# Performance work log

Measured on AMD Instinct MI355X. Metric: run time of the kernel, lower is better.

## Reference

```python
import jax, jax.numpy as jnp
import numpy as np

N, E, D, H, C = 20000, 320000, 128, 4, 128
NEG_SLOPE = 0.2

def _ln(x, g, b, eps=1e-5):
    mu = x.mean(-1, keepdims=True)
    var = ((x - mu) ** 2).mean(-1, keepdims=True)
    return (x - mu) * jax.lax.rsqrt(var + eps) * g + b

def _gatv2(x, src, dst, Wl, bl, Wr, br, att, b):
    # PyG GATv2Conv, concat=False (mean over heads), dropout off (eval)
    n = x.shape[0]
    xl = (x @ Wl + bl).reshape(n, H, C)   # source transform
    xr = (x @ Wr + br).reshape(n, H, C)   # destination transform
    e = jax.nn.leaky_relu(xl[src] + xr[dst], NEG_SLOPE)      # [E,H,C]
    score = jnp.einsum('ehc,hc->eh', e, att)                 # [E,H]
    m = jax.ops.segment_max(score, dst, num_segments=n)      # per-dst max
    w = jnp.exp(score - m[dst])
    denom = jax.ops.segment_sum(w, dst, num_segments=n)
    alpha = w / (denom[dst] + 1e-16)                         # softmax over incoming edges
    out = jax.ops.segment_sum(alpha[:, :, None] * xl[src], dst, num_segments=n)  # [N,H,C]
    return out.mean(axis=1) + b

def setup_inputs() -> dict:
    key = jax.random.key(0)
    ks = jax.random.split(key, 34)
    s = 1.0 / np.sqrt(D)
    def w(k, shape):
        return jax.random.normal(k, shape, jnp.float32) * s
    inp = {
        'x': jax.random.normal(ks[0], (N, D), jnp.float32),
        'edge_index': jax.random.randint(ks[1], (2, E), 0, N, jnp.int32),
        'W_in': w(ks[2], (D, C)), 'b_in': jnp.zeros((C,), jnp.float32),
        'c1_Wl': w(ks[3], (C, H * C)), 'c1_bl': jnp.zeros((H * C,), jnp.float32),
        'c1_Wr': w(ks[4], (C, H * C)), 'c1_br': jnp.zeros((H * C,), jnp.float32),
        'c1_att': w(ks[5], (H, C)), 'c1_b': jnp.zeros((C,), jnp.float32),
        'ln1_g': jnp.ones((C,), jnp.float32), 'ln1_b': jnp.zeros((C,), jnp.float32),
        'a_Wl': w(ks[6], (C, H * C)), 'a_bl': jnp.zeros((H * C,), jnp.float32),
        'a_Wr': w(ks[7], (C, H * C)), 'a_br': jnp.zeros((H * C,), jnp.float32),
        'a_att': w(ks[8], (H, C)), 'a_b': jnp.zeros((C,), jnp.float32),
        'aln_g': jnp.ones((C,), jnp.float32), 'aln_b': jnp.zeros((C,), jnp.float32),
        'ah_W': w(ks[9], (C, 1)), 'ah_b': jnp.zeros((1,), jnp.float32),
        'k_Wl': w(ks[10], (C, H * C)), 'k_bl': jnp.zeros((H * C,), jnp.float32),
        'k_Wr': w(ks[11], (C, H * C)), 'k_br': jnp.zeros((H * C,), jnp.float32),
        'k_att': w(ks[12], (H, C)), 'k_b': jnp.zeros((C,), jnp.float32),
        'kln_g': jnp.ones((C,), jnp.float32), 'kln_b': jnp.zeros((C,), jnp.float32),
        'kh_W': w(ks[13], (C, 1)), 'kh_b': jnp.zeros((1,), jnp.float32),
    }
    return inp

def reference(x, edge_index, W_in, b_in,
              c1_Wl, c1_bl, c1_Wr, c1_br, c1_att, c1_b, ln1_g, ln1_b,
              a_Wl, a_bl, a_Wr, a_br, a_att, a_b, aln_g, aln_b, ah_W, ah_b,
              k_Wl, k_bl, k_Wr, k_br, k_att, k_b, kln_g, kln_b, kh_W, kh_b):
    n = x.shape[0]
    loops = jnp.arange(n, dtype=edge_index.dtype)
    src = jnp.concatenate([edge_index[0], loops])  # PyG adds self-loops by default
    dst = jnp.concatenate([edge_index[1], loops])
    h = jax.nn.relu(x @ W_in + b_in)
    h_res = _gatv2(h, src, dst, c1_Wl, c1_bl, c1_Wr, c1_br, c1_att, c1_b)
    h = jax.nn.relu(_ln(h + h_res, ln1_g, ln1_b))
    xa = _gatv2(h, src, dst, a_Wl, a_bl, a_Wr, a_br, a_att, a_b)
    xa = jax.nn.relu(_ln(xa + h, aln_g, aln_b))
    action_logits = (xa @ ah_W + ah_b).squeeze(-1)
    xc = _gatv2(h, src, dst, k_Wl, k_bl, k_Wr, k_br, k_att, k_b)
    xc = jax.nn.relu(_ln(xc + h, kln_g, kln_b))
    state_value = xc @ kh_W + kh_b
    return action_logits, state_value
```

## Files before the change

### kernel.cpp

```cpp
#include <hip/hip_runtime.h>
#include <hip/hip_bf16.h>

typedef __hip_bfloat16 bf16;
typedef __attribute__((ext_vector_type(8))) short short8;
typedef __attribute__((ext_vector_type(4))) short short4_t;
typedef __attribute__((ext_vector_type(4))) float float4_t;
typedef __attribute__((ext_vector_type(2))) float float2v;
typedef __attribute__((ext_vector_type(2))) unsigned int uint2v;

__device__ __forceinline__ short f2bs(float f) {
    bf16 b = __float2bfloat16(f);
    return *(short*)&b;
}

template <int CTRL>
__device__ __forceinline__ float dpp_addf(float x) {
    int s = __builtin_amdgcn_update_dpp(
        0, __builtin_bit_cast(int, x), CTRL, 0xf, 0xf, true);
    return x + __builtin_bit_cast(float, s);
}
__device__ __forceinline__ float rowsum16(float x) {
    x = dpp_addf<0xB1>(x);
    x = dpp_addf<0x4E>(x);
    x = dpp_addf<0x141>(x);
    x = dpp_addf<0x140>(x);
    return x;
}

__global__ __launch_bounds__(256) void zero_kernel(int* __restrict__ a, int n) {
    int i = blockIdx.x * 256 + threadIdx.x;
    if (i < n) a[i] = 0;
}

__global__ __launch_bounds__(256) void count_kernel(const int* __restrict__ ei,
                                                    int* __restrict__ cnt, int E, int N) {
    int e = blockIdx.x * 256 + threadIdx.x;
    if (e >= E + N) return;
    int d = (e < E) ? ei[(size_t)E + e] : (e - E);
    atomicAdd(&cnt[d], 1);
}

__global__ __launch_bounds__(1024) void scan_kernel(const int* __restrict__ cnt,
                                                    int* __restrict__ rowptr, int N) {
    __shared__ int ps[1024];
    const int tid = threadIdx.x;
    const int chunk = (N + 1023) / 1024;
    const int base = tid * chunk;
    int s = 0;
    for (int i = 0; i < chunk; ++i) { int j = base + i; if (j < N) s += cnt[j]; }
    ps[tid] = s;
    __syncthreads();
    for (int off = 1; off < 1024; off <<= 1) {
        int v = (tid >= off) ? ps[tid - off] : 0;
        __syncthreads();
        ps[tid] += v;
        __syncthreads();
    }
    int run = (tid == 0) ? 0 : ps[tid - 1];
    for (int i = 0; i < chunk; ++i) {
        int j = base + i;
        if (j < N) { rowptr[j] = run; run += cnt[j]; }
    }
    if (tid == 1023) rowptr[N] = run;
}

__global__ __launch_bounds__(256) void scatter_kernel(const int* __restrict__ ei,
                                                      const int* __restrict__ rowptr,
                                                      int* __restrict__ cursor,
                                                      int* __restrict__ csr_off,
                                                      int E, int N) {
    int e = blockIdx.x * 256 + threadIdx.x;
    if (e >= E + N) return;
    int s, d;
    if (e < E) { s = ei[e]; d = ei[(size_t)E + e]; }
    else       { s = e - E; d = e - E; }
    int pos = atomicAdd(&cursor[d], 1);
    csr_off[rowptr[d] + pos] = s * 4096;
}

__global__ __launch_bounds__(256) void transpose_w_kernel(
        const float* __restrict__ W_in,
        const float* __restrict__ c1_Wl, const float* __restrict__ c1_Wr,
        const float* __restrict__ a_Wl, const float* __restrict__ a_Wr,
        const float* __restrict__ k_Wl, const float* __restrict__ k_Wr,
        bf16* __restrict__ Wt) {
    __shared__ float tile[32][33];
    const float* src; int nc, drow;
    switch (blockIdx.z) {
        case 0: src = W_in;  nc = 128; drow = 0;    break;
        case 1: src = c1_Wl; nc = 512; drow = 128;  break;
        case 2: src = c1_Wr; nc = 512; drow = 640;  break;
        case 3: src = a_Wl;  nc = 512; drow = 1152; break;
        case 4: src = a_Wr;  nc = 512; drow = 1664; break;
        case 5: src = k_Wl;  nc = 512; drow = 2176; break;
        default: src = k_Wr; nc = 512; drow = 2688; break;
    }
    const int n0 = blockIdx.x * 32;
    if (n0 >= nc) return;
    const int k0 = blockIdx.y * 32;
    const int tx = threadIdx.x & 31, ty = threadIdx.x >> 5;
#pragma unroll
    for (int i = 0; i < 4; ++i)
        tile[ty + i * 8][tx] = src[(size_t)(k0 + ty + i * 8) * nc + n0 + tx];
    __syncthreads();
#pragma unroll
    for (int i = 0; i < 4; ++i)
        Wt[(size_t)(drow + n0 + ty + i * 8) * 128 + k0 + tx] =
            __float2bfloat16(tile[tx][ty + i * 8]);
}

__global__ __launch_bounds__(256) void bias_kernel(
        const float* __restrict__ c1_bl, const float* __restrict__ c1_br,
        const float* __restrict__ a_bl, const float* __restrict__ a_br,
        const float* __restrict__ k_bl, const float* __restrict__ k_br,
        float* __restrict__ b1, float* __restrict__ bak) {
    int i = blockIdx.x * 256 + threadIdx.x;
    if (i < 1024) {
        b1[i] = (i < 512) ? c1_bl[i] : c1_br[i - 512];
    } else if (i < 3072) {
        int j = i - 1024;
        const float* b = (j < 512) ? a_bl : (j < 1024) ? a_br : (j < 1536) ? k_bl : k_br;
        bak[j] = b[j & 511];
    }
}

__global__ __launch_bounds__(256, 2) void gemm_mfma_kernel(
        const float* __restrict__ A, const bf16* __restrict__ Ab,
        const bf16* __restrict__ Wt,
        const float* __restrict__ bias,
        float* __restrict__ outF, bf16* __restrict__ outB,
        int M, int ldc, int relu) {
    __shared__ short As[128][136];
    __shared__ short Bs[128][136];
    const int tid = threadIdx.x;
    const int m0 = blockIdx.x * 128;
    const int n0 = blockIdx.y * 128;

    if (Ab) {
        short8 zero8;
#pragma unroll
        for (int q = 0; q < 8; ++q) zero8[q] = 0;
#pragma unroll
        for (int i = 0; i < 8; ++i) {
            int idx = i * 256 + tid;
            int r = idx >> 4, k8 = (idx & 15) * 8;
            int gm = m0 + r;
            short8 s = (gm < M) ? *(const short8*)&Ab[(size_t)gm * 128 + k8] : zero8;
            *(short8*)&As[r][k8] = s;
        }
    } else {
#pragma unroll
        for (int i = 0; i < 16; ++i) {
            int idx = i * 256 + tid;
            int r = idx >> 5, k4 = (idx & 31) * 4;
            int gm = m0 + r;
            float4 v = (gm < M) ? *(const float4*)&A[(size_t)gm * 128 + k4]
                                : make_float4(0.f, 0.f, 0.f, 0.f);
            short4_t s;
            s.x = f2bs(v.x); s.y = f2bs(v.y); s.z = f2bs(v.z); s.w = f2bs(v.w);
            *(short4_t*)&As[r][k4] = s;
        }
    }
#pragma unroll
    for (int i = 0; i < 8; ++i) {
        int idx = i * 256 + tid;
        int nr = idx >> 4, k8 = (idx & 15) * 8;
        *(short8*)&Bs[nr][k8] = *(const short8*)&Wt[(size_t)(n0 + nr) * 128 + k8];
    }
    __syncthreads();

    const int lane = tid & 63;
    const int w = tid >> 6;
    const int wm = (w >> 1) * 64, wn = (w & 1) * 64;
    const int fr = lane & 15;
    const int fq = (lane >> 4) * 8;

    float4_t acc[4][4] = {};
#pragma unroll
    for (int kk = 0; kk < 128; kk += 32) {
        short8 a[4], b[4];
#pragma unroll
        for (int t = 0; t < 4; ++t) a[t] = *(const short8*)&As[wm + t * 16 + fr][kk + fq];
#pragma unroll
        for (int t = 0; t < 4; ++t) b[t] = *(const short8*)&Bs[wn + t * 16 + fr][kk + fq];
#pragma unroll
        for (int ti = 0; ti < 4; ++ti)
#pragma unroll
            for (int tj = 0; tj < 4; ++tj)
                acc[ti][tj] = __builtin_amdgcn_mfma_f32_16x16x32_bf16(
                    a[ti], b[tj], acc[ti][tj], 0, 0, 0);
    }

    const int r0 = (lane >> 4) * 4;
#pragma unroll
    for (int ti = 0; ti < 4; ++ti) {
#pragma unroll
        for (int tj = 0; tj < 4; ++tj) {
            int col = n0 + wn + tj * 16 + fr;
            float bz = bias[col];
#pragma unroll
            for (int r = 0; r < 4; ++r) {
                size_t row = m0 + wm + ti * 16 + r0 + r;
                float v = acc[ti][tj][r] + bz;
                if (relu) v = fmaxf(v, 0.f);
                if (outF) outF[row * ldc + col] = v;
                if (outB) outB[row * ldc + col] = __float2bfloat16(v);
            }
        }
    }
}

__global__ __launch_bounds__(256) void gat_kernel(
        const bf16* __restrict__ xl, const bf16* __restrict__ xr,
        const float* __restrict__ att,
        const int* __restrict__ rowptr, const int* __restrict__ csr_off,
        const float* __restrict__ h_res,
        const float* __restrict__ gbias,
        const float* __restrict__ ln_g, const float* __restrict__ ln_b,
        float* __restrict__ h_out, bf16* __restrict__ h_outb,
        const float* __restrict__ head_W, const float* __restrict__ head_b,
        float* __restrict__ out_scalar, int mode, int N) {
    const int n = blockIdx.x * 4 + (threadIdx.x >> 6);
    if (n >= N) return;
    const int lane = threadIdx.x & 63;
    const int sl = lane & 15;
    const int hc = (lane >> 4) * 128 + sl * 8;

    float2v c1[4], c2[4], xr2[4];
    {
        const float* ap = att + hc;
        short8 v = *(const short8*)(xr + (size_t)n * 2048 + hc);
        const unsigned int* uv = (const unsigned int*)&v;
#pragma unroll
        for (int j = 0; j < 4; ++j) {
            float a0 = ap[2 * j], a1 = ap[2 * j + 1];
            c1[j].x = 0.6f * a0; c1[j].y = 0.6f * a1;
            c2[j].x = 0.4f * a0; c2[j].y = 0.4f * a1;
            unsigned u = uv[j];
            xr2[j].x = __uint_as_float(u << 16);
            xr2[j].y = __uint_as_float(u & 0xffff0000u);
        }
    }
    const int rs = rowptr[n], re = rowptr[n + 1];
    const char* xlh = (const char*)xl + (size_t)hc * 2;

    float l = 0.f;
    float2v acc2[4] = {};
    int o0 = csr_off[rs];
    short8 va = *(const short8*)(xlh + o0);
    int o1 = (rs + 1 < re) ? csr_off[rs + 1] : o0;
    short8 vb = *(const short8*)(xlh + o1);
    int o2 = (rs + 2 < re) ? csr_off[rs + 2] : o0;

    for (int e = rs; e < re; ++e) {
        short8 cur = va; va = vb;
        if (e + 2 < re) {
            vb = *(const short8*)(xlh + o2);
            o2 = (e + 3 < re) ? csr_off[e + 3] : o0;
        }
        const unsigned int* uv = (const unsigned int*)&cur;
        float2v pa = {0.f, 0.f}, pb = {0.f, 0.f};
        float2v xs[4];
#pragma unroll
        for (int j = 0; j < 4; ++j) {
            unsigned u = uv[j];
            float2v x;
            x.x = __uint_as_float(u << 16);
            x.y = __uint_as_float(u & 0xffff0000u);
            xs[j] = x;
            float2v t = x + xr2[j];
            float2v ta = __builtin_bit_cast(float2v,
                           __builtin_bit_cast(uint2v, t) & 0x7fffffffu);
            pa = __builtin_elementwise_fma(c1[j], t, pa);
            pb = __builtin_elementwise_fma(c2[j], ta, pb);
        }
        float p = rowsum16((pa.x + pb.x) + (pa.y + pb.y));
        float wv = __expf(fminf(p, 60.f));
        l += wv;
        float2v ws = {wv, wv};
#pragma unroll
        for (int j = 0; j < 4; ++j)
            acc2[j] = __builtin_elementwise_fma(ws, xs[j], acc2[j]);
    }

    float* accf = (float*)acc2;
    const float inv = 0.25f / (l + 1e-16f);
#pragma unroll
    for (int j = 0; j < 8; ++j) accf[j] *= inv;
#pragma unroll
    for (int off = 16; off <= 32; off <<= 1)
#pragma unroll
        for (int j = 0; j < 8; ++j) accf[j] += __shfl_xor(accf[j], off, 64);

    if (lane < 16) {
        const int cb = sl * 8;
        const float* hr = h_res + (size_t)n * 128 + cb;
        float vv[8];
#pragma unroll
        for (int j = 0; j < 8; ++j) vv[j] = accf[j] + gbias[cb + j] + hr[j];
        float t1 = 0.f, t2 = 0.f;
#pragma unroll
        for (int j = 0; j < 8; ++j) { t1 += vv[j]; t2 += vv[j] * vv[j]; }
        const float s1 = rowsum16(t1), s2 = rowsum16(t2);
        const float mu   = s1 * 0.0078125f;
        const float var  = s2 * 0.0078125f - mu * mu;
        const float rstd = rsqrtf(var + 1e-5f);
        float y[8];
#pragma unroll
        for (int j = 0; j < 8; ++j) {
            y[j] = fmaf((vv[j] - mu) * rstd, ln_g[cb + j], ln_b[cb + j]);
            y[j] = fmaxf(y[j], 0.f);
        }
        if (mode == 0) {
            float4 y0 = make_float4(y[0], y[1], y[2], y[3]);
            float4 y1 = make_float4(y[4], y[5], y[6], y[7]);
            *(float4*)(h_out + (size_t)n * 128 + cb) = y0;
            *(float4*)(h_out + (size_t)n * 128 + cb + 4) = y1;
            short8 yb;
#pragma unroll
            for (int j = 0; j < 8; ++j) yb[j] = f2bs(y[j]);
            *(short8*)(h_outb + (size_t)n * 128 + cb) = yb;
        } else {
            float d = 0.f;
#pragma unroll
            for (int j = 0; j < 8; ++j) d += y[j] * head_W[cb + j];
            d = rowsum16(d);
            if (lane == 0) out_scalar[n] = d + head_b[0];
        }
    }
}

extern "C" void kernel_launch(void* const* d_in, const int* in_sizes, int n_in,
                              void* d_out, int out_size, void* d_ws, size_t ws_size,
                              hipStream_t stream) {
    const float* x      = (const float*)d_in[0];
    const int*   ei     = (const int*)  d_in[1];
    const float* W_in   = (const float*)d_in[2];
    const float* b_in   = (const float*)d_in[3];
    const float* c1_Wl  = (const float*)d_in[4];
    const float* c1_bl  = (const float*)d_in[5];
    const float* c1_Wr  = (const float*)d_in[6];
    const float* c1_br  = (const float*)d_in[7];
    const float* c1_att = (const float*)d_in[8];
    const float* c1_b   = (const float*)d_in[9];
    const float* ln1_g  = (const float*)d_in[10];
    const float* ln1_b  = (const float*)d_in[11];
    const float* a_Wl   = (const float*)d_in[12];
    const float* a_bl   = (const float*)d_in[13];
    const float* a_Wr   = (const float*)d_in[14];
    const float* a_br   = (const float*)d_in[15];
    const float* a_att  = (const float*)d_in[16];
    const float* a_b    = (const float*)d_in[17];
    const float* aln_g  = (const float*)d_in[18];
    const float* aln_b  = (const float*)d_in[19];
    const float* ah_W   = (const float*)d_in[20];
    const float* ah_b   = (const float*)d_in[21];
    const float* k_Wl   = (const float*)d_in[22];
    const float* k_bl   = (const float*)d_in[23];
    const float* k_Wr   = (const float*)d_in[24];
    const float* k_br   = (const float*)d_in[25];
    const float* k_att  = (const float*)d_in[26];
    const float* k_b    = (const float*)d_in[27];
    const float* kln_g  = (const float*)d_in[28];
    const float* kln_b  = (const float*)d_in[29];
    const float* kh_W   = (const float*)d_in[30];
    const float* kh_b   = (const float*)d_in[31];

    const int N  = in_sizes[0] / 128;
    const int E  = in_sizes[1] / 2;
    const int ET = E + N;
    const int MB = (N + 127) / 128;
    const int Npad = MB * 128;

    char* ws = (char*)d_ws;
    size_t off = 0;
    auto alloc = [&](size_t bytes) -> void* {
        void* p = ws + off;
        off += (bytes + 255) & ~(size_t)255;
        return p;
    };
    int*   rowptr  = (int*)alloc((size_t)(N + 1) * 4);
    int*   cntcur  = (int*)alloc((size_t)2 * N * 4);
    int*   csr_off = (int*)alloc((size_t)ET * 4);
    float* h0      = (float*)alloc((size_t)Npad * 128 * 4);
    bf16*  h0b     = (bf16*)alloc((size_t)Npad * 128 * 2);
    float* h1      = (float*)alloc((size_t)Npad * 128 * 4);
    bf16*  h1b     = (bf16*)alloc((size_t)Npad * 128 * 2);
    bf16*  Wt      = (bf16*)alloc((size_t)3200 * 128 * 2);
    float* b1cat   = (float*)alloc(1024 * 4);
    float* bakcat  = (float*)alloc(2048 * 4);
    bf16*  cat     = (bf16*)alloc((size_t)Npad * 2048 * 2);

    int* cnt    = cntcur;
    int* cursor = cntcur + N;
    const bf16* Wt_in = Wt;
    const bf16* Wt_1  = Wt + 128 * 128;
    const bf16* Wt_ak = Wt + 128 * 128 + 1024 * 128;

    float* out_logits = (float*)d_out;
    float* out_value  = (float*)d_out + N;

    zero_kernel<<<(2 * N + 255) / 256, 256, 0, stream>>>(cntcur, 2 * N);
    count_kernel<<<(ET + 255) / 256, 256, 0, stream>>>(ei, cnt, E, N);
    transpose_w_kernel<<<dim3(16, 4, 7), 256, 0, stream>>>(
        W_in, c1_Wl, c1_Wr, a_Wl, a_Wr, k_Wl, k_Wr, Wt);
    bias_kernel<<<12, 256, 0, stream>>>(c1_bl, c1_br, a_bl, a_br, k_bl, k_br, b1cat, bakcat);
    scan_kernel<<<1, 1024, 0, stream>>>(cnt, rowptr, N);
    scatter_kernel<<<(ET + 255) / 256, 256, 0, stream>>>(ei, rowptr, cursor, csr_off, E, N);

    gemm_mfma_kernel<<<dim3(MB, 1), 256, 0, stream>>>(x, nullptr, Wt_in, b_in,
                                                      h0, h0b, N, 128, 1);
    gemm_mfma_kernel<<<dim3(MB, 8), 256, 0, stream>>>(nullptr, h0b, Wt_1, b1cat,
                                                      nullptr, cat, Npad, 2048, 0);
    gat_kernel<<<(N + 3) / 4, 256, 0, stream>>>(cat, cat + 512, c1_att, rowptr, csr_off,
                                      h0, c1_b, ln1_g, ln1_b, h1, h1b,
                                      nullptr, nullptr, nullptr, 0, N);
    gemm_mfma_kernel<<<dim3(MB, 16), 256, 0, stream>>>(nullptr, h1b, Wt_ak, bakcat,
                                                       nullptr, cat, Npad, 2048, 0);
    gat_kernel<<<(N + 3) / 4, 256, 0, stream>>>(cat, cat + 512, a_att, rowptr, csr_off,
                                      h1, a_b, aln_g, aln_b, nullptr, nullptr,
                                      ah_W, ah_b, out_logits, 1, N);
    gat_kernel<<<(N + 3) / 4, 256, 0, stream>>>(cat + 1024, cat + 1536, k_att, rowptr, csr_off,
                                      h1, k_b, kln_g, kln_b, nullptr, nullptr,
                                      kh_W, kh_b, out_value, 1, N);
}
```

Measured before the change: 419.6 us.

## Fuse actor and critic GAT aggregations into one kernel sharing CSR traversal

Replaces the two separate actor and critic GAT launches with a single gat2 kernel. It walks each node's incoming edges once, gathering both the actor and critic source features and running both softmax aggregations plus their LayerNorm and heads. It also folds the bias-concat kernel into the weight-transpose launch and simplifies the leaky-ReLU coefficient math. The aim is to cut the repeated CSR and h_res reads and one launch, at the cost of roughly double register pressure per thread in the fused loop.

```diff
diff --git a/kernel.cpp b/kernel.cpp
--- a/kernel.cpp
+++ b/kernel.cpp
@@ -83,7 +83,25 @@
         const float* __restrict__ c1_Wl, const float* __restrict__ c1_Wr,
         const float* __restrict__ a_Wl, const float* __restrict__ a_Wr,
         const float* __restrict__ k_Wl, const float* __restrict__ k_Wr,
-        bf16* __restrict__ Wt) {
+        bf16* __restrict__ Wt,
+        const float* __restrict__ c1_bl, const float* __restrict__ c1_br,
+        const float* __restrict__ a_bl, const float* __restrict__ a_br,
+        const float* __restrict__ k_bl, const float* __restrict__ k_br,
+        float* __restrict__ b1, float* __restrict__ bak) {
+    if (blockIdx.z == 7) {
+        int flat = blockIdx.y * 16 + blockIdx.x;
+        if (flat >= 12) return;
+        int i = flat * 256 + threadIdx.x;
+        if (i < 1024) {
+            b1[i] = (i < 512) ? c1_bl[i] : c1_br[i - 512];
+        } else if (i < 3072) {
+            int j = i - 1024;
+            const float* b = (j < 512) ? a_bl : (j < 1024) ? a_br
+                           : (j < 1536) ? k_bl : k_br;
+            bak[j] = b[j & 511];
+        }
+        return;
+    }
     __shared__ float tile[32][33];
     const float* src; int nc, drow;
     switch (blockIdx.z) {
@@ -107,21 +125,6 @@
     for (int i = 0; i < 4; ++i)
         Wt[(size_t)(drow + n0 + ty + i * 8) * 128 + k0 + tx] =
             __float2bfloat16(tile[tx][ty + i * 8]);
-}
-
-__global__ __launch_bounds__(256) void bias_kernel(
-        const float* __restrict__ c1_bl, const float* __restrict__ c1_br,
-        const float* __restrict__ a_bl, const float* __restrict__ a_br,
-        const float* __restrict__ k_bl, const float* __restrict__ k_br,
-        float* __restrict__ b1, float* __restrict__ bak) {
-    int i = blockIdx.x * 256 + threadIdx.x;
-    if (i < 1024) {
-        b1[i] = (i < 512) ? c1_bl[i] : c1_br[i - 512];
-    } else if (i < 3072) {
-        int j = i - 1024;
-        const float* b = (j < 512) ? a_bl : (j < 1024) ? a_br : (j < 1536) ? k_bl : k_br;
-        bak[j] = b[j & 511];
-    }
 }
 
 __global__ __launch_bounds__(256, 2) void gemm_mfma_kernel(
@@ -217,25 +220,21 @@
         const float* __restrict__ h_res,
         const float* __restrict__ gbias,
         const float* __restrict__ ln_g, const float* __restrict__ ln_b,
-        float* __restrict__ h_out, bf16* __restrict__ h_outb,
-        const float* __restrict__ head_W, const float* __restrict__ head_b,
-        float* __restrict__ out_scalar, int mode, int N) {
+        float* __restrict__ h_out, bf16* __restrict__ h_outb, int N) {
     const int n = blockIdx.x * 4 + (threadIdx.x >> 6);
     if (n >= N) return;
     const int lane = threadIdx.x & 63;
     const int sl = lane & 15;
     const int hc = (lane >> 4) * 128 + sl * 8;
 
-    float2v c1[4], c2[4], xr2[4];
+    float2v a2[4], xr2[4];
     {
         const float* ap = att + hc;
         short8 v = *(const short8*)(xr + (size_t)n * 2048 + hc);
         const unsigned int* uv = (const unsigned int*)&v;
 #pragma unroll
         for (int j = 0; j < 4; ++j) {
-            float a0 = ap[2 * j], a1 = ap[2 * j + 1];
-            c1[j].x = 0.6f * a0; c1[j].y = 0.6f * a1;
-            c2[j].x = 0.4f * a0; c2[j].y = 0.4f * a1;
+            a2[j].x = ap[2 * j]; a2[j].y = ap[2 * j + 1];
             unsigned u = uv[j];
             xr2[j].x = __uint_as_float(u << 16);
             xr2[j].y = __uint_as_float(u & 0xffff0000u);
@@ -271,10 +270,10 @@
             float2v t = x + xr2[j];
             float2v ta = __builtin_bit_cast(float2v,
                            __builtin_bit_cast(uint2v, t) & 0x7fffffffu);
-            pa = __builtin_elementwise_fma(c1[j], t, pa);
-            pb = __builtin_elementwise_fma(c2[j], ta, pb);
-        }
-        float p = rowsum16((pa.x + pb.x) + (pa.y + pb.y));
+            pa = __builtin_elementwise_fma(a2[j], t, pa);
+            pb = __builtin_elementwise_fma(a2[j], ta, pb);
+        }
+        float p = rowsum16(0.6f * (pa.x + pa.y) + 0.4f * (pb.x + pb.y));
         float wv = __expf(fminf(p, 60.f));
         l += wv;
         float2v ws = {wv, wv};
@@ -311,21 +310,172 @@
             y[j] = fmaf((vv[j] - mu) * rstd, ln_g[cb + j], ln_b[cb + j]);
             y[j] = fmaxf(y[j], 0.f);
         }
-        if (mode == 0) {
-            float4 y0 = make_float4(y[0], y[1], y[2], y[3]);
-            float4 y1 = make_float4(y[4], y[5], y[6], y[7]);
-            *(float4*)(h_out + (size_t)n * 128 + cb) = y0;
-            *(float4*)(h_out + (size_t)n * 128 + cb + 4) = y1;
-            short8 yb;
-#pragma unroll
-            for (int j = 0; j < 8; ++j) yb[j] = f2bs(y[j]);
-            *(short8*)(h_outb + (size_t)n * 128 + cb) = yb;
+        *(float4*)(h_out + (size_t)n * 128 + cb) = make_float4(y[0], y[1], y[2], y[3]);
+        *(float4*)(h_out + (size_t)n * 128 + cb + 4) = make_float4(y[4], y[5], y[6], y[7]);
+        short8 yb;
+#pragma unroll
+        for (int j = 0; j < 8; ++j) yb[j] = f2bs(y[j]);
+        *(short8*)(h_outb + (size_t)n * 128 + cb) = yb;
+    }
+}
+
+__global__ __launch_bounds__(256) void gat2_kernel(
+        const bf16* __restrict__ cat,
+        const float* __restrict__ a_att, const float* __restrict__ k_att,
+        const int* __restrict__ rowptr, const int* __restrict__ csr_off,
+        const float* __restrict__ h_res,
+        const float* __restrict__ a_gb, const float* __restrict__ k_gb,
+        const float* __restrict__ aln_g, const float* __restrict__ aln_b,
+        const float* __restrict__ kln_g, const float* __restrict__ kln_b,
+        const float* __restrict__ ah_W, const float* __restrict__ ah_b,
+        const float* __restrict__ kh_W, const float* __restrict__ kh_b,
+        float* __restrict__ out_logits, float* __restrict__ out_value, int N) {
+    const int n = blockIdx.x * 4 + (threadIdx.x >> 6);
+    if (n >= N) return;
+    const int lane = threadIdx.x & 63;
+    const int sl = lane & 15;
+    const int hc = (lane >> 4) * 128 + sl * 8;
+
+    float2v aa[4], ak[4], xra[4], xrk[4];
+    {
+        const float* apa = a_att + hc;
+        const float* apk = k_att + hc;
+        short8 vra = *(const short8*)(cat + (size_t)n * 2048 + 512 + hc);
+        short8 vrk = *(const short8*)(cat + (size_t)n * 2048 + 1536 + hc);
+        const unsigned int* ua = (const unsigned int*)&vra;
+        const unsigned int* uk = (const unsigned int*)&vrk;
+#pragma unroll
+        for (int j = 0; j < 4; ++j) {
+            aa[j].x = apa[2 * j]; aa[j].y = apa[2 * j + 1];
+            ak[j].x = apk[2 * j]; ak[j].y = apk[2 * j + 1];
+            unsigned u = ua[j];
+            xra[j].x = __uint_as_float(u << 16);
+            xra[j].y = __uint_as_float(u & 0xffff0000u);
+            u = uk[j];
+            xrk[j].x = __uint_as_float(u << 16);
+            xrk[j].y = __uint_as_float(u & 0xffff0000u);
+        }
+    }
+    const int rs = rowptr[n], re = rowptr[n + 1];
+    const char* xlh = (const char*)cat + (size_t)hc * 2;
+
+    float la = 0.f, lk = 0.f;
+    float2v acca[4] = {}, acck[4] = {};
+    int o0 = csr_off[rs];
+    short8 vaa = *(const short8*)(xlh + o0);
+    short8 vak = *(const short8*)(xlh + o0 + 2048);
+    int o1 = (rs + 1 < re) ? csr_off[rs + 1] : o0;
+    short8 vba = *(const short8*)(xlh + o1);
+    short8 vbk = *(const short8*)(xlh + o1 + 2048);
+    int o2 = (rs + 2 < re) ? csr_off[rs + 2] : o0;
+
+    for (int e = rs; e < re; ++e) {
+        short8 ca = vaa, ck = vak;
+        vaa = vba; vak = vbk;
+        if (e + 2 < re) {
+            vba = *(const short8*)(xlh + o2);
+            vbk = *(const short8*)(xlh + o2 + 2048);
+            o2 = (e + 3 < re) ? csr_off[e + 3] : o0;
+        }
+        const unsigned int* ua = (const unsigned int*)&ca;
+        const unsigned int* uk = (const unsigned int*)&ck;
+        float2v paa = {0.f, 0.f}, pba = {0.f, 0.f};
+        float2v pak = {0.f, 0.f}, pbk = {0.f, 0.f};
+        float2v xsa[4], xsk[4];
+#pragma unroll
+        for (int j = 0; j < 4; ++j) {
+            unsigned u = ua[j];
+            float2v x;
+            x.x = __uint_as_float(u << 16);
+            x.y = __uint_as_float(u & 0xffff0000u);
+            xsa[j] = x;
+            float2v t = x + xra[j];
+            float2v ta = __builtin_bit_cast(float2v,
+                           __builtin_bit_cast(uint2v, t) & 0x7fffffffu);
+            paa = __builtin_elementwise_fma(aa[j], t, paa);
+            pba = __builtin_elementwise_fma(aa[j], ta, pba);
+
+            u = uk[j];
+            x.x = __uint_as_float(u << 16);
+            x.y = __uint_as_float(u & 0xffff0000u);
+            xsk[j] = x;
+            t = x + xrk[j];
+            ta = __builtin_bit_cast(float2v,
+                   __builtin_bit_cast(uint2v, t) & 0x7fffffffu);
+            pak = __builtin_elementwise_fma(ak[j], t, pak);
+            pbk = __builtin_elementwise_fma(ak[j], ta, pbk);
+        }
+        float p_a = rowsum16(0.6f * (paa.x + paa.y) + 0.4f * (pba.x + pba.y));
+        float p_k = rowsum16(0.6f * (pak.x + pak.y) + 0.4f * (pbk.x + pbk.y));
+        float wa = __expf(fminf(p_a, 60.f));
+        float wk = __expf(fminf(p_k, 60.f));
+        la += wa; lk += wk;
+        float2v wsa = {wa, wa}, wsk = {wk, wk};
+#pragma unroll
+        for (int j = 0; j < 4; ++j) {
+            acca[j] = __builtin_elementwise_fma(wsa, xsa[j], acca[j]);
+            acck[j] = __builtin_elementwise_fma(wsk, xsk[j], acck[j]);
+        }
+    }
+
+    float* afa = (float*)acca;
+    float* afk = (float*)acck;
+    const float inva = 0.25f / (la + 1e-16f);
+    const float invk = 0.25f / (lk + 1e-16f);
+#pragma unroll
+    for (int j = 0; j < 8; ++j) { afa[j] *= inva; afk[j] *= invk; }
+#pragma unroll
+    for (int off = 16; off <= 32; off <<= 1)
+#pragma unroll
+        for (int j = 0; j < 8; ++j) {
+            afa[j] += __shfl_xor(afa[j], off, 64);
+            afk[j] += __shfl_xor(afk[j], off, 64);
+        }
+
+    if (lane < 32) {
+        const int cb = sl * 8;
+        const float* hr = h_res + (size_t)n * 128 + cb;
+        float hrv[8];
+#pragma unroll
+        for (int j = 0; j < 8; ++j) hrv[j] = hr[j];
+        if (lane < 16) {
+            float vv[8];
+#pragma unroll
+            for (int j = 0; j < 8; ++j) vv[j] = afa[j] + a_gb[cb + j] + hrv[j];
+            float t1 = 0.f, t2 = 0.f;
+#pragma unroll
+            for (int j = 0; j < 8; ++j) { t1 += vv[j]; t2 += vv[j] * vv[j]; }
+            const float s1 = rowsum16(t1), s2 = rowsum16(t2);
+            const float mu   = s1 * 0.0078125f;
+            const float var  = s2 * 0.0078125f - mu * mu;
+            const float rstd = rsqrtf(var + 1e-5f);
+            float d = 0.f;
+#pragma unroll
+            for (int j = 0; j < 8; ++j) {
+                float y = fmaf((vv[j] - mu) * rstd, aln_g[cb + j], aln_b[cb + j]);
+                d += fmaxf(y, 0.f) * ah_W[cb + j];
+            }
+            d = rowsum16(d);
+            if (sl == 0) out_logits[n] = d + ah_b[0];
         } else {
+            float vv[8];
+#pragma unroll
+            for (int j = 0; j < 8; ++j) vv[j] = afk[j] + k_gb[cb + j] + hrv[j];
+            float t1 = 0.f, t2 = 0.f;
+#pragma unroll
+            for (int j = 0; j < 8; ++j) { t1 += vv[j]; t2 += vv[j] * vv[j]; }
+            const float s1 = rowsum16(t1), s2 = rowsum16(t2);
+            const float mu   = s1 * 0.0078125f;
+            const float var  = s2 * 0.0078125f - mu * mu;
+            const float rstd = rsqrtf(var + 1e-5f);
             float d = 0.f;
 #pragma unroll
-            for (int j = 0; j < 8; ++j) d += y[j] * head_W[cb + j];
+            for (int j = 0; j < 8; ++j) {
+                float y = fmaf((vv[j] - mu) * rstd, kln_g[cb + j], kln_b[cb + j]);
+                d += fmaxf(y, 0.f) * kh_W[cb + j];
+            }
             d = rowsum16(d);
-            if (lane == 0) out_scalar[n] = d + head_b[0];
+            if (sl == 0) out_value[n] = d + kh_b[0];
         }
     }
 }
@@ -402,9 +552,9 @@
 
     zero_kernel<<<(2 * N + 255) / 256, 256, 0, stream>>>(cntcur, 2 * N);
     count_kernel<<<(ET + 255) / 256, 256, 0, stream>>>(ei, cnt, E, N);
-    transpose_w_kernel<<<dim3(16, 4, 7), 256, 0, stream>>>(
-        W_in, c1_Wl, c1_Wr, a_Wl, a_Wr, k_Wl, k_Wr, Wt);
-    bias_kernel<<<12, 256, 0, stream>>>(c1_bl, c1_br, a_bl, a_br, k_bl, k_br, b1cat, bakcat);
+    transpose_w_kernel<<<dim3(16, 4, 8), 256, 0, stream>>>(
+        W_in, c1_Wl, c1_Wr, a_Wl, a_Wr, k_Wl, k_Wr, Wt,
+        c1_bl, c1_br, a_bl, a_br, k_bl, k_br, b1cat, bakcat);
     scan_kernel<<<1, 1024, 0, stream>>>(cnt, rowptr, N);
     scatter_kernel<<<(ET + 255) / 256, 256, 0, stream>>>(ei, rowptr, cursor, csr_off, E, N);
 
@@ -413,14 +563,11 @@
     gemm_mfma_kernel<<<dim3(MB, 8), 256, 0, stream>>>(nullptr, h0b, Wt_1, b1cat,
                                                       nullptr, cat, Npad, 2048, 0);
     gat_kernel<<<(N + 3) / 4, 256, 0, stream>>>(cat, cat + 512, c1_att, rowptr, csr_off,
-                                      h0, c1_b, ln1_g, ln1_b, h1, h1b,
-                                      nullptr, nullptr, nullptr, 0, N);
+                                      h0, c1_b, ln1_g, ln1_b, h1, h1b, N);
     gemm_mfma_kernel<<<dim3(MB, 16), 256, 0, stream>>>(nullptr, h1b, Wt_ak, bakcat,
                                                        nullptr, cat, Npad, 2048, 0);
-    gat_kernel<<<(N + 3) / 4, 256, 0, stream>>>(cat, cat + 512, a_att, rowptr, csr_off,
-                                      h1, a_b, aln_g, aln_b, nullptr, nullptr,
-                                      ah_W, ah_b, out_logits, 1, N);
-    gat_kernel<<<(N + 3) / 4, 256, 0, stream>>>(cat + 1024, cat + 1536, k_att, rowptr, csr_off,
-                                      h1, k_b, kln_g, kln_b, nullptr, nullptr,
-                                      kh_W, kh_b, out_value, 1, N);
-}
+    gat2_kernel<<<(N + 3) / 4, 256, 0, stream>>>(cat, a_att, k_att, rowptr, csr_off,
+                                      h1, a_b, k_b, aln_g, aln_b, kln_g, kln_b,
+                                      ah_W, ah_b, kh_W, kh_b,
+                                      out_logits, out_value, N);
+}
```

New measurement: 411.9 us. No clear change (-1.8%).

## Fuse actor/critic GAT kernels, unroll edge loop by two, merge bias setup

Applied to the files above, without the earlier changes.

Merges the two final GAT launches (actor and critic) into one kernel where paired wavefronts handle the two networks for the same node, sharing rowptr/csr reads and neighbour locality. Rewrites the edge loop to process two edges per step with a deeper four-edge prefetch, giving more memory-level parallelism, and moves the 0.6/0.4 attention scaling to after the reduction. Folds the bias-concatenation kernel into the weight transpose launch to save one launch. The unrolled loop raises register pressure and adds a masked extra edge when the degree is odd.

```diff
diff --git a/kernel.cpp b/kernel.cpp
--- a/kernel.cpp
+++ b/kernel.cpp
@@ -83,7 +83,25 @@
         const float* __restrict__ c1_Wl, const float* __restrict__ c1_Wr,
         const float* __restrict__ a_Wl, const float* __restrict__ a_Wr,
         const float* __restrict__ k_Wl, const float* __restrict__ k_Wr,
-        bf16* __restrict__ Wt) {
+        bf16* __restrict__ Wt,
+        const float* __restrict__ c1_bl, const float* __restrict__ c1_br,
+        const float* __restrict__ a_bl, const float* __restrict__ a_br,
+        const float* __restrict__ k_bl, const float* __restrict__ k_br,
+        float* __restrict__ b1, float* __restrict__ bak) {
+    if (blockIdx.z == 7) {
+        int flat = blockIdx.y * 16 + blockIdx.x;
+        if (flat >= 12) return;
+        int i = flat * 256 + threadIdx.x;
+        if (i < 1024) {
+            b1[i] = (i < 512) ? c1_bl[i] : c1_br[i - 512];
+        } else if (i < 3072) {
+            int j = i - 1024;
+            const float* b = (j < 512) ? a_bl : (j < 1024) ? a_br
+                           : (j < 1536) ? k_bl : k_br;
+            bak[j] = b[j & 511];
+        }
+        return;
+    }
     __shared__ float tile[32][33];
     const float* src; int nc, drow;
     switch (blockIdx.z) {
@@ -107,21 +125,6 @@
     for (int i = 0; i < 4; ++i)
         Wt[(size_t)(drow + n0 + ty + i * 8) * 128 + k0 + tx] =
             __float2bfloat16(tile[tx][ty + i * 8]);
-}
-
-__global__ __launch_bounds__(256) void bias_kernel(
-        const float* __restrict__ c1_bl, const float* __restrict__ c1_br,
-        const float* __restrict__ a_bl, const float* __restrict__ a_br,
-        const float* __restrict__ k_bl, const float* __restrict__ k_br,
-        float* __restrict__ b1, float* __restrict__ bak) {
-    int i = blockIdx.x * 256 + threadIdx.x;
-    if (i < 1024) {
-        b1[i] = (i < 512) ? c1_bl[i] : c1_br[i - 512];
-    } else if (i < 3072) {
-        int j = i - 1024;
-        const float* b = (j < 512) ? a_bl : (j < 1024) ? a_br : (j < 1536) ? k_bl : k_br;
-        bak[j] = b[j & 511];
-    }
 }
 
 __global__ __launch_bounds__(256, 2) void gemm_mfma_kernel(
@@ -210,6 +213,91 @@
     }
 }
 
+__device__ __forceinline__ void gat_process2(
+        short8 v0, short8 v1, int e, int re,
+        const float2v a2[4], const float2v xr2[4],
+        float2v acc2[4], float& l) {
+    const unsigned int* u0 = (const unsigned int*)&v0;
+    const unsigned int* u1 = (const unsigned int*)&v1;
+    float2v pa0 = {0.f, 0.f}, pb0 = {0.f, 0.f};
+    float2v pa1 = {0.f, 0.f}, pb1 = {0.f, 0.f};
+    float2v xs0[4], xs1[4];
+#pragma unroll
+    for (int j = 0; j < 4; ++j) {
+        unsigned u = u0[j];
+        float2v x;
+        x.x = __uint_as_float(u << 16);
+        x.y = __uint_as_float(u & 0xffff0000u);
+        xs0[j] = x;
+        float2v t = x + xr2[j];
+        float2v ta = __builtin_bit_cast(float2v,
+                       __builtin_bit_cast(uint2v, t) & 0x7fffffffu);
+        pa0 = __builtin_elementwise_fma(a2[j], t, pa0);
+        pb0 = __builtin_elementwise_fma(a2[j], ta, pb0);
+
+        u = u1[j];
+        x.x = __uint_as_float(u << 16);
+        x.y = __uint_as_float(u & 0xffff0000u);
+        xs1[j] = x;
+        t = x + xr2[j];
+        ta = __builtin_bit_cast(float2v,
+               __builtin_bit_cast(uint2v, t) & 0x7fffffffu);
+        pa1 = __builtin_elementwise_fma(a2[j], t, pa1);
+        pb1 = __builtin_elementwise_fma(a2[j], ta, pb1);
+    }
+    float p0 = rowsum16(0.6f * (pa0.x + pa0.y) + 0.4f * (pb0.x + pb0.y));
+    float p1 = rowsum16(0.6f * (pa1.x + pa1.y) + 0.4f * (pb1.x + pb1.y));
+    float w0 = __expf(fminf(p0, 60.f));
+    float w1 = (e + 1 < re) ? __expf(fminf(p1, 60.f)) : 0.f;
+    l += w0 + w1;
+    float2v ws0 = {w0, w0}, ws1 = {w1, w1};
+#pragma unroll
+    for (int j = 0; j < 4; ++j) {
+        acc2[j] = __builtin_elementwise_fma(ws0, xs0[j], acc2[j]);
+        acc2[j] = __builtin_elementwise_fma(ws1, xs1[j], acc2[j]);
+    }
+}
+
+__device__ __forceinline__ void gat_edge_loop(
+        const char* __restrict__ xlh, const int* __restrict__ csr_off,
+        int rs, int re,
+        const float2v a2[4], const float2v xr2[4],
+        float2v acc2[4], float& l) {
+    int i1 = (rs + 1 < re) ? rs + 1 : rs;
+    int i2 = (rs + 2 < re) ? rs + 2 : rs;
+    int i3 = (rs + 3 < re) ? rs + 3 : rs;
+    int oA0 = csr_off[rs], oA1 = csr_off[i1];
+    short8 vA0 = *(const short8*)(xlh + oA0);
+    short8 vA1 = *(const short8*)(xlh + oA1);
+    int oB0 = csr_off[i2], oB1 = csr_off[i3];
+    short8 vB0 = *(const short8*)(xlh + oB0);
+    short8 vB1 = *(const short8*)(xlh + oB1);
+
+    int e = rs;
+    for (;;) {
+        {
+            int j0 = (e + 4 < re) ? e + 4 : rs;
+            int j1 = (e + 5 < re) ? e + 5 : rs;
+            int n0 = csr_off[j0], n1 = csr_off[j1];
+            gat_process2(vA0, vA1, e, re, a2, xr2, acc2, l);
+            vA0 = *(const short8*)(xlh + n0);
+            vA1 = *(const short8*)(xlh + n1);
+        }
+        e += 2;
+        if (e >= re) break;
+        {
+            int j0 = (e + 4 < re) ? e + 4 : rs;
+            int j1 = (e + 5 < re) ? e + 5 : rs;
+            int n0 = csr_off[j0], n1 = csr_off[j1];
+            gat_process2(vB0, vB1, e, re, a2, xr2, acc2, l);
+            vB0 = *(const short8*)(xlh + n0);
+            vB1 = *(const short8*)(xlh + n1);
+        }
+        e += 2;
+        if (e >= re) break;
+    }
+}
+
 __global__ __launch_bounds__(256) void gat_kernel(
         const bf16* __restrict__ xl, const bf16* __restrict__ xr,
         const float* __restrict__ att,
@@ -217,25 +305,21 @@
         const float* __restrict__ h_res,
         const float* __restrict__ gbias,
         const float* __restrict__ ln_g, const float* __restrict__ ln_b,
-        float* __restrict__ h_out, bf16* __restrict__ h_outb,
-        const float* __restrict__ head_W, const float* __restrict__ head_b,
-        float* __restrict__ out_scalar, int mode, int N) {
+        float* __restrict__ h_out, bf16* __restrict__ h_outb, int N) {
     const int n = blockIdx.x * 4 + (threadIdx.x >> 6);
     if (n >= N) return;
     const int lane = threadIdx.x & 63;
     const int sl = lane & 15;
     const int hc = (lane >> 4) * 128 + sl * 8;
 
-    float2v c1[4], c2[4], xr2[4];
+    float2v a2[4], xr2[4];
     {
         const float* ap = att + hc;
         short8 v = *(const short8*)(xr + (size_t)n * 2048 + hc);
         const unsigned int* uv = (const unsigned int*)&v;
 #pragma unroll
         for (int j = 0; j < 4; ++j) {
-            float a0 = ap[2 * j], a1 = ap[2 * j + 1];
-            c1[j].x = 0.6f * a0; c1[j].y = 0.6f * a1;
-            c2[j].x = 0.4f * a0; c2[j].y = 0.4f * a1;
+            a2[j].x = ap[2 * j]; a2[j].y = ap[2 * j + 1];
             unsigned u = uv[j];
             xr2[j].x = __uint_as_float(u << 16);
             xr2[j].y = __uint_as_float(u & 0xffff0000u);
@@ -246,42 +330,7 @@
 
     float l = 0.f;
     float2v acc2[4] = {};
-    int o0 = csr_off[rs];
-    short8 va = *(const short8*)(xlh + o0);
-    int o1 = (rs + 1 < re) ? csr_off[rs + 1] : o0;
-    short8 vb = *(const short8*)(xlh + o1);
-    int o2 = (rs + 2 < re) ? csr_off[rs + 2] : o0;
-
-    for (int e = rs; e < re; ++e) {
-        short8 cur = va; va = vb;
-        if (e + 2 < re) {
-            vb = *(const short8*)(xlh + o2);
-            o2 = (e + 3 < re) ? csr_off[e + 3] : o0;
-        }
-        const unsigned int* uv = (const unsigned int*)&cur;
-        float2v pa = {0.f, 0.f}, pb = {0.f, 0.f};
-        float2v xs[4];
-#pragma unroll
-        for (int j = 0; j < 4; ++j) {
-            unsigned u = uv[j];
-            float2v x;
-            x.x = __uint_as_float(u << 16);
-            x.y = __uint_as_float(u & 0xffff0000u);
-            xs[j] = x;
-            float2v t = x + xr2[j];
-            float2v ta = __builtin_bit_cast(float2v,
-                           __builtin_bit_cast(uint2v, t) & 0x7fffffffu);
-            pa = __builtin_elementwise_fma(c1[j], t, pa);
-            pb = __builtin_elementwise_fma(c2[j], ta, pb);
-        }
-        float p = rowsum16((pa.x + pb.x) + (pa.y + pb.y));
-        float wv = __expf(fminf(p, 60.f));
-        l += wv;
-        float2v ws = {wv, wv};
-#pragma unroll
-        for (int j = 0; j < 4; ++j)
-            acc2[j] = __builtin_elementwise_fma(ws, xs[j], acc2[j]);
-    }
+    gat_edge_loop(xlh, csr_off, rs, re, a2, xr2, acc2, l);
 
     float* accf = (float*)acc2;
     const float inv = 0.25f / (l + 1e-16f);
@@ -311,22 +360,93 @@
             y[j] = fmaf((vv[j] - mu) * rstd, ln_g[cb + j], ln_b[cb + j]);
             y[j] = fmaxf(y[j], 0.f);
         }
-        if (mode == 0) {
-            float4 y0 = make_float4(y[0], y[1], y[2], y[3]);
-            float4 y1 = make_float4(y[4], y[5], y[6], y[7]);
-            *(float4*)(h_out + (size_t)n * 128 + cb) = y0;
-            *(float4*)(h_out + (size_t)n * 128 + cb + 4) = y1;
-            short8 yb;
-#pragma unroll
-            for (int j = 0; j < 8; ++j) yb[j] = f2bs(y[j]);
-            *(short8*)(h_outb + (size_t)n * 128 + cb) = yb;
-        } else {
-            float d = 0.f;
-#pragma unroll
-            for (int j = 0; j < 8; ++j) d += y[j] * head_W[cb + j];
-            d = rowsum16(d);
-            if (lane == 0) out_scalar[n] = d + head_b[0];
-        }
+        *(float4*)(h_out + (size_t)n * 128 + cb) = make_float4(y[0], y[1], y[2], y[3]);
+        *(float4*)(h_out + (size_t)n * 128 + cb + 4) = make_float4(y[4], y[5], y[6], y[7]);
+        short8 yb;
+#pragma unroll
+        for (int j = 0; j < 8; ++j) yb[j] = f2bs(y[j]);
+        *(short8*)(h_outb + (size_t)n * 128 + cb) = yb;
+    }
+}
+
+__global__ __launch_bounds__(256) void gat2_kernel(
+        const bf16* __restrict__ cat,
+        const float* __restrict__ a_att, const float* __restrict__ k_att,
+        const int* __restrict__ rowptr, const int* __restrict__ csr_off,
+        const float* __restrict__ h_res,
+        const float* __restrict__ a_gb, const float* __restrict__ k_gb,
+        const float* __restrict__ aln_g, const float* __restrict__ aln_b,
+        const float* __restrict__ kln_g, const float* __restrict__ kln_b,
+        const float* __restrict__ ah_W, const float* __restrict__ ah_b,
+        const float* __restrict__ kh_W, const float* __restrict__ kh_b,
+        float* __restrict__ out_logits, float* __restrict__ out_value, int N) {
+    const int w = threadIdx.x >> 6;
+    const int n = blockIdx.x * 2 + (w >> 1);
+    if (n >= N) return;
+    const int net = w & 1;
+    const int lane = threadIdx.x & 63;
+    const int sl = lane & 15;
+    const int hc = (lane >> 4) * 128 + sl * 8;
+    const int colbase = net ? 1024 : 0;
+
+    const float* att  = net ? k_att : a_att;
+    const float* gb   = net ? k_gb  : a_gb;
+    const float* lg   = net ? kln_g : aln_g;
+    const float* lb   = net ? kln_b : aln_b;
+    const float* hW   = net ? kh_W  : ah_W;
+    const float* hb   = net ? kh_b  : ah_b;
+    float* outp       = net ? out_value : out_logits;
+
+    float2v a2[4], xr2[4];
+    {
+        const float* ap = att + hc;
+        short8 v = *(const short8*)(cat + (size_t)n * 2048 + colbase + 512 + hc);
+        const unsigned int* uv = (const unsigned int*)&v;
+#pragma unroll
+        for (int j = 0; j < 4; ++j) {
+            a2[j].x = ap[2 * j]; a2[j].y = ap[2 * j + 1];
+            unsigned u = uv[j];
+            xr2[j].x = __uint_as_float(u << 16);
+            xr2[j].y = __uint_as_float(u & 0xffff0000u);
+        }
+    }
+    const int rs = rowptr[n], re = rowptr[n + 1];
+    const char* xlh = (const char*)cat + (size_t)(colbase + hc) * 2;
+
+    float l = 0.f;
+    float2v acc2[4] = {};
+    gat_edge_loop(xlh, csr_off, rs, re, a2, xr2, acc2, l);
+
+    float* accf = (float*)acc2;
+    const float inv = 0.25f / (l + 1e-16f);
+#pragma unroll
+    for (int j = 0; j < 8; ++j) accf[j] *= inv;
+#pragma unroll
+    for (int off = 16; off <= 32; off <<= 1)
+#pragma unroll
+        for (int j = 0; j < 8; ++j) accf[j] += __shfl_xor(accf[j], off, 64);
+
+    if (lane < 16) {
+        const int cb = sl * 8;
+        const float* hr = h_res + (size_t)n * 128 + cb;
+        float vv[8];
+#pragma unroll
+        for (int j = 0; j < 8; ++j) vv[j] = accf[j] + gb[cb + j] + hr[j];
+        float t1 = 0.f, t2 = 0.f;
+#pragma unroll
+        for (int j = 0; j < 8; ++j) { t1 += vv[j]; t2 += vv[j] * vv[j]; }
+        const float s1 = rowsum16(t1), s2 = rowsum16(t2);
+        const float mu   = s1 * 0.0078125f;
+        const float var  = s2 * 0.0078125f - mu * mu;
+        const float rstd = rsqrtf(var + 1e-5f);
+        float d = 0.f;
+#pragma unroll
+        for (int j = 0; j < 8; ++j) {
+            float y = fmaf((vv[j] - mu) * rstd, lg[cb + j], lb[cb + j]);
+            d += fmaxf(y, 0.f) * hW[cb + j];
+        }
+        d = rowsum16(d);
+        if (sl == 0) outp[n] = d + hb[0];
     }
 }
 
@@ -402,9 +522,9 @@
 
     zero_kernel<<<(2 * N + 255) / 256, 256, 0, stream>>>(cntcur, 2 * N);
     count_kernel<<<(ET + 255) / 256, 256, 0, stream>>>(ei, cnt, E, N);
-    transpose_w_kernel<<<dim3(16, 4, 7), 256, 0, stream>>>(
-        W_in, c1_Wl, c1_Wr, a_Wl, a_Wr, k_Wl, k_Wr, Wt);
-    bias_kernel<<<12, 256, 0, stream>>>(c1_bl, c1_br, a_bl, a_br, k_bl, k_br, b1cat, bakcat);
+    transpose_w_kernel<<<dim3(16, 4, 8), 256, 0, stream>>>(
+        W_in, c1_Wl, c1_Wr, a_Wl, a_Wr, k_Wl, k_Wr, Wt,
+        c1_bl, c1_br, a_bl, a_br, k_bl, k_br, b1cat, bakcat);
     scan_kernel<<<1, 1024, 0, stream>>>(cnt, rowptr, N);
     scatter_kernel<<<(ET + 255) / 256, 256, 0, stream>>>(ei, rowptr, cursor, csr_off, E, N);
 
@@ -413,14 +533,11 @@
     gemm_mfma_kernel<<<dim3(MB, 8), 256, 0, stream>>>(nullptr, h0b, Wt_1, b1cat,
                                                       nullptr, cat, Npad, 2048, 0);
     gat_kernel<<<(N + 3) / 4, 256, 0, stream>>>(cat, cat + 512, c1_att, rowptr, csr_off,
-                                      h0, c1_b, ln1_g, ln1_b, h1, h1b,
-                                      nullptr, nullptr, nullptr, 0, N);
+                                      h0, c1_b, ln1_g, ln1_b, h1, h1b, N);
     gemm_mfma_kernel<<<dim3(MB, 16), 256, 0, stream>>>(nullptr, h1b, Wt_ak, bakcat,
                                                        nullptr, cat, Npad, 2048, 0);
-    gat_kernel<<<(N + 3) / 4, 256, 0, stream>>>(cat, cat + 512, a_att, rowptr, csr_off,
-                                      h1, a_b, aln_g, aln_b, nullptr, nullptr,
-                                      ah_W, ah_b, out_logits, 1, N);
-    gat_kernel<<<(N + 3) / 4, 256, 0, stream>>>(cat + 1024, cat + 1536, k_att, rowptr, csr_off,
-                                      h1, k_b, kln_g, kln_b, nullptr, nullptr,
-                                      kh_W, kh_b, out_value, 1, N);
-}
+    gat2_kernel<<<(N + 1) / 2, 256, 0, stream>>>(cat, a_att, k_att, rowptr, csr_off,
+                                      h1, a_b, k_b, aln_g, aln_b, kln_g, kln_b,
+                                      ah_W, ah_b, kh_W, kh_b,
+                                      out_logits, out_value, N);
+}
```

Result: no change. 420.5 us (+0.2%).
